# Performance work log

Hardware: AMD Instinct MI355X
Metric: run time of the kernel (lower is better)

Reference implementation:

```python
import jax, jax.numpy as jnp
import numpy as np

N_NODES = 100000
N_EDGES = 1600000
D_FEAT = 64


def setup_inputs() -> dict:
    key = jax.random.key(0)
    k1, k2, k3 = jax.random.split(key, 3)
    h = jax.random.normal(k1, (N_NODES, D_FEAT), dtype=jnp.float32)
    src = jax.random.randint(k2, (N_EDGES,), 0, N_NODES, dtype=jnp.int32)
    dst = jax.random.randint(k3, (N_EDGES,), 0, N_NODES, dtype=jnp.int32)
    edge_index = jnp.stack([src, dst], axis=0)  # [2, E]
    return {"h": h, "edge_index": edge_index}


def reference(h, edge_index):
    # EdgePassing: message = src node features (gather along edges)
    # Max_aggregation: per-dst-node max over incoming messages (segment max)
    src, dst = edge_index[0], edge_index[1]
    msgs = h[src]  # [E, D] gathered mailbox, never densified per-node
    agg = jax.ops.segment_max(msgs, dst, num_segments=N_NODES)  # [N, D]
    # DGL leaves nodes with no incoming messages at zero; segment_max yields -inf
    return jnp.where(jnp.isneginf(agg), jnp.zeros_like(agg), agg)
```

## Files before the change

### kernel.cpp

```cpp
#include <hip/hip_runtime.h>
#include <stdint.h>

#define D_FEAT 64
#define NEG_INF_BITS 0xFF800000u
#define ENC_NEG_INF  0x007FFFFFu
#define NPB 64
#define BSHIFT 6
#define BM_BLOCK 256
#define MAXB 2048
#define PL_BLOCKS 256
#define PL_THREADS 1024
#define O_CAP 65536

__device__ __forceinline__ unsigned enc_f32(float v) {
    unsigned b = __float_as_uint(v);
    return ((int)b >= 0) ? (b ^ 0x80000000u) : ~b;
}
__device__ __forceinline__ unsigned dec_bits(unsigned u) {
    if (u == ENC_NEG_INF) return 0u;
    return (u & 0x80000000u) ? (u ^ 0x80000000u) : ~u;
}

__global__ void __launch_bounds__(PL_THREADS)
place_kernel(const int* __restrict__ src, const int* __restrict__ dst,
             int* __restrict__ cnt, int* __restrict__ ovf_cnt,
             int* __restrict__ ovf_dst, int* __restrict__ ovf_src,
             unsigned* __restrict__ packed,
             int E, int Te, int B, int cap, int aligned4) {
    __shared__ int lh[MAXB];
    int t = blockIdx.x;
    int beg = t * Te;
    int end = min(E, beg + Te);
    if (beg >= end) return;
    for (int i = threadIdx.x; i < B; i += blockDim.x) lh[i] = 0;
    __syncthreads();
    int nE = end - beg;
    int n4 = aligned4 ? (nE >> 2) : 0;
    const int4* d4 = (const int4*)(dst + beg);
    for (int k = threadIdx.x; k < n4; k += blockDim.x) {
        int4 d = d4[k];
        atomicAdd(&lh[d.x >> BSHIFT], 1);
        atomicAdd(&lh[d.y >> BSHIFT], 1);
        atomicAdd(&lh[d.z >> BSHIFT], 1);
        atomicAdd(&lh[d.w >> BSHIFT], 1);
    }
    for (int i = beg + (n4 << 2) + threadIdx.x; i < end; i += blockDim.x)
        atomicAdd(&lh[dst[i] >> BSHIFT], 1);
    __syncthreads();
    for (int i = threadIdx.x; i < B; i += blockDim.x) {
        int c = lh[i];
        lh[i] = c ? atomicAdd(&cnt[i], c) : 0;
    }
    __syncthreads();
    for (int i = beg + threadIdx.x; i < end; i += blockDim.x) {
        int d = dst[i];
        int s = src[i];
        int b = d >> BSHIFT;
        int pos = atomicAdd(&lh[b], 1);
        if (pos < cap) {
            packed[(size_t)b * cap + pos] = (unsigned)s | ((unsigned)(d & (NPB - 1)) << 17);
        } else {
            int o = atomicAdd(ovf_cnt, 1);
            if (o < O_CAP) { ovf_dst[o] = d; ovf_src[o] = s; }
        }
    }
}

__global__ void __launch_bounds__(BM_BLOCK)
bucket_max_kernel(const float* __restrict__ h,
                  const int* __restrict__ cnt, const int* __restrict__ ovf_cnt,
                  const int* __restrict__ ovf_dst, const int* __restrict__ ovf_src,
                  const int* __restrict__ src, const int* __restrict__ dst,
                  const unsigned* __restrict__ packed,
                  float* __restrict__ out, int N, int E, int cap) {
    __shared__ unsigned buf[NPB * D_FEAT];
    int b = blockIdx.x;
    int tid = threadIdx.x;
    int node0 = b << BSHIFT;
    int nvals = (min(NPB, N - node0)) * D_FEAT;

    for (int i = tid; i < NPB * D_FEAT; i += BM_BLOCK) buf[i] = ENC_NEG_INF;
    __syncthreads();

    int total = cnt[b];
    int beg = b * cap;
    int end = beg + min(total, cap);
    int wid = tid >> 6;
    int lane = tid & 63;

    for (int base = beg + (wid << 6); base < end; base += BM_BLOCK) {
        int nk = min(64, end - base);
        unsigned p = (lane < nk) ? packed[base + lane] : 0u;
        int j = 0;
        for (; j + 8 <= nk; j += 8) {
            unsigned q[8];
            float v[8];
            #pragma unroll
            for (int k = 0; k < 8; ++k) q[k] = (unsigned)__shfl((int)p, j + k);
            #pragma unroll
            for (int k = 0; k < 8; ++k) v[k] = h[(size_t)(q[k] & 0x1FFFFu) * D_FEAT + lane];
            #pragma unroll
            for (int k = 0; k < 8; ++k)
                atomicMax(&buf[(q[k] >> 17) * D_FEAT + lane], enc_f32(v[k]));
        }
        for (; j < nk; ++j) {
            unsigned pj = (unsigned)__shfl((int)p, j);
            float v = h[(size_t)(pj & 0x1FFFFu) * D_FEAT + lane];
            atomicMax(&buf[(pj >> 17) * D_FEAT + lane], enc_f32(v));
        }
    }

    int ov = *ovf_cnt;
    if (ov > 0) {
        if (ov <= O_CAP) {
            for (int i = 0; i < ov; ++i) {
                int d = ovf_dst[i];
                if ((d >> BSHIFT) == b) {
                    float v = h[(size_t)ovf_src[i] * D_FEAT + lane];
                    atomicMax(&buf[(d & (NPB - 1)) * D_FEAT + lane], enc_f32(v));
                }
            }
        } else if (total > cap) {
            for (int e = tid; e < E; e += BM_BLOCK) {
                int d = dst[e];
                if ((d >> BSHIFT) == b) {
                    const float* hr = h + (size_t)src[e] * D_FEAT;
                    int row = (d & (NPB - 1)) * D_FEAT;
                    for (int f = 0; f < D_FEAT; ++f)
                        atomicMax(&buf[row + f], enc_f32(hr[f]));
                }
            }
        }
    }
    __syncthreads();

    if (nvals == NPB * D_FEAT) {
        uint4* o4 = (uint4*)(out + (size_t)node0 * D_FEAT);
        const uint4* b4 = (const uint4*)buf;
        for (int i = tid; i < (NPB * D_FEAT) / 4; i += BM_BLOCK) {
            uint4 u = b4[i];
            uint4 r;
            r.x = dec_bits(u.x); r.y = dec_bits(u.y);
            r.z = dec_bits(u.z); r.w = dec_bits(u.w);
            o4[i] = r;
        }
    } else {
        unsigned* o = (unsigned*)(out + (size_t)node0 * D_FEAT);
        for (int i = tid; i < nvals; i += BM_BLOCK) o[i] = dec_bits(buf[i]);
    }
}

__global__ void init_out_kernel(uint4* __restrict__ out, int n4) {
    int i = blockIdx.x * blockDim.x + threadIdx.x;
    if (i < n4) {
        uint4 v;
        v.x = NEG_INF_BITS; v.y = NEG_INF_BITS; v.z = NEG_INF_BITS; v.w = NEG_INF_BITS;
        out[i] = v;
    }
}
__global__ void scatter_max_kernel(const float* __restrict__ h, const int* __restrict__ src,
                                   const int* __restrict__ dst, float* __restrict__ out, int E) {
    int gid = blockIdx.x * blockDim.x + threadIdx.x;
    int e = gid >> 6;
    if (e >= E) return;
    int lane = gid & 63;
    float v = h[src[e] * D_FEAT + lane];
    int* addr = (int*)(out + dst[e] * D_FEAT + lane);
    if (v >= 0.0f) atomicMax(addr, __float_as_int(v));
    else           atomicMin((unsigned int*)addr, __float_as_uint(v));
}
__global__ void finalize_kernel(float* __restrict__ out, int n) {
    int i = blockIdx.x * blockDim.x + threadIdx.x;
    if (i < n && __float_as_uint(out[i]) == NEG_INF_BITS) out[i] = 0.0f;
}

extern "C" void kernel_launch(void* const* d_in, const int* in_sizes, int n_in,
                              void* d_out, int out_size, void* d_ws, size_t ws_size,
                              hipStream_t stream) {
    const float* h = (const float*)d_in[0];
    const int* edge_index = (const int*)d_in[1];
    int E = in_sizes[1] / 2;
    const int* src = edge_index;
    const int* dst = edge_index + E;
    float* out = (float*)d_out;
    int N = out_size / D_FEAT;

    int B = (N + NPB - 1) >> BSHIFT;

    int cap = 0;
    if (B > 0) {
        cap = (((E / B) * 5) / 4 + 63) & ~63;
        if (cap < 128) cap = 128;
    }
    size_t need = ((size_t)B + 1 + 2 * (size_t)O_CAP + (size_t)B * cap) * sizeof(int);

    if (N <= (1 << 17) && B <= MAXB && E > 0 && cap > 0 && ws_size >= need) {
        int* cnt         = (int*)d_ws;
        int* ovf_cnt     = cnt + B;
        int* ovf_dst     = ovf_cnt + 1;
        int* ovf_src     = ovf_dst + O_CAP;
        unsigned* packed = (unsigned*)(ovf_src + O_CAP);

        int aligned4 = (((((uintptr_t)dst) | ((uintptr_t)src)) & 15) == 0) ? 1 : 0;

        hipMemsetAsync(cnt, 0, (size_t)(B + 1) * sizeof(int), stream);

        int Te = ((E + PL_BLOCKS - 1) / PL_BLOCKS + 3) & ~3;
        place_kernel<<<PL_BLOCKS, PL_THREADS, 0, stream>>>(
            src, dst, cnt, ovf_cnt, ovf_dst, ovf_src, packed, E, Te, B, cap, aligned4);

        bucket_max_kernel<<<B, BM_BLOCK, 0, stream>>>(
            h, cnt, ovf_cnt, ovf_dst, ovf_src, src, dst, packed, out, N, E, cap);
    } else {
        int n4 = out_size / 4;
        init_out_kernel<<<(n4 + 255) / 256, 256, 0, stream>>>((uint4*)out, n4);
        long long total = (long long)E * 64;
        scatter_max_kernel<<<(int)((total + 255) / 256), 256, 0, stream>>>(h, src, dst, out, E);
        finalize_kernel<<<(out_size + 255) / 256, 256, 0, stream>>>(out, out_size);
    }
}
```

Baseline: 155.8 us.

## Pad per-block bucket reservations to 16 entries and cut placement blocks to 64

Each placement block now reserves bucket slots rounded up to multiples of 16 and fills the unused tail with a sentinel. Writes into the packed edge list therefore land in aligned, contiguous 64-byte runs per block rather than scattered single words. Using fewer placement blocks (64 instead of 256) keeps the padding overhead bounded, and the bucket capacity is enlarged to absorb it. The max kernel skips sentinel entries. The cost is more workspace, extra sentinel writes, a branch in the hot gather loop, and less parallelism in the placement pass.

Result: slower. 234.5 us (+50.5%).

```diff
diff --git a/kernel.cpp b/kernel.cpp
--- a/kernel.cpp
+++ b/kernel.cpp
@@ -4,11 +4,14 @@
 #define D_FEAT 64
 #define NEG_INF_BITS 0xFF800000u
 #define ENC_NEG_INF  0x007FFFFFu
+#define SENTINEL     0xFFFFFFFFu
 #define NPB 64
 #define BSHIFT 6
 #define BM_BLOCK 256
 #define MAXB 2048
-#define PL_BLOCKS 256
+#define PAD 16
+#define PL_BLOCKS_PAD 64
+#define PL_BLOCKS_STD 256
 #define PL_THREADS 1024
 #define O_CAP 65536
 
@@ -26,42 +29,58 @@
              int* __restrict__ cnt, int* __restrict__ ovf_cnt,
              int* __restrict__ ovf_dst, int* __restrict__ ovf_src,
              unsigned* __restrict__ packed,
-             int E, int Te, int B, int cap, int aligned4) {
-    __shared__ int lh[MAXB];
+             int E, int Te, int B, int cap, int aligned4, int pad) {
+    __shared__ int lcnt[MAXB];
+    __shared__ int lcur[MAXB];
     int t = blockIdx.x;
     int beg = t * Te;
     int end = min(E, beg + Te);
     if (beg >= end) return;
-    for (int i = threadIdx.x; i < B; i += blockDim.x) lh[i] = 0;
+    for (int i = threadIdx.x; i < B; i += blockDim.x) lcnt[i] = 0;
     __syncthreads();
     int nE = end - beg;
     int n4 = aligned4 ? (nE >> 2) : 0;
     const int4* d4 = (const int4*)(dst + beg);
     for (int k = threadIdx.x; k < n4; k += blockDim.x) {
         int4 d = d4[k];
-        atomicAdd(&lh[d.x >> BSHIFT], 1);
-        atomicAdd(&lh[d.y >> BSHIFT], 1);
-        atomicAdd(&lh[d.z >> BSHIFT], 1);
-        atomicAdd(&lh[d.w >> BSHIFT], 1);
+        atomicAdd(&lcnt[d.x >> BSHIFT], 1);
+        atomicAdd(&lcnt[d.y >> BSHIFT], 1);
+        atomicAdd(&lcnt[d.z >> BSHIFT], 1);
+        atomicAdd(&lcnt[d.w >> BSHIFT], 1);
     }
     for (int i = beg + (n4 << 2) + threadIdx.x; i < end; i += blockDim.x)
-        atomicAdd(&lh[dst[i] >> BSHIFT], 1);
+        atomicAdd(&lcnt[dst[i] >> BSHIFT], 1);
     __syncthreads();
     for (int i = threadIdx.x; i < B; i += blockDim.x) {
-        int c = lh[i];
-        lh[i] = c ? atomicAdd(&cnt[i], c) : 0;
+        int c = lcnt[i];
+        int res = (pad > 1) ? ((c + pad - 1) & ~(pad - 1)) : c;
+        lcur[i] = c ? atomicAdd(&cnt[i], res) : 0;
     }
     __syncthreads();
     for (int i = beg + threadIdx.x; i < end; i += blockDim.x) {
         int d = dst[i];
         int s = src[i];
         int b = d >> BSHIFT;
-        int pos = atomicAdd(&lh[b], 1);
+        int pos = atomicAdd(&lcur[b], 1);
         if (pos < cap) {
             packed[(size_t)b * cap + pos] = (unsigned)s | ((unsigned)(d & (NPB - 1)) << 17);
         } else {
             int o = atomicAdd(ovf_cnt, 1);
             if (o < O_CAP) { ovf_dst[o] = d; ovf_src[o] = s; }
+        }
+    }
+    if (pad > 1) {
+        __syncthreads();
+        for (int i = threadIdx.x; i < B; i += blockDim.x) {
+            int c = lcnt[i];
+            if (c) {
+                int curv = lcur[i];
+                int base = curv - c;
+                int endp = base + ((c + pad - 1) & ~(pad - 1));
+                int fe = min(endp, cap);
+                for (int s2 = curv; s2 < fe; ++s2)
+                    packed[(size_t)i * cap + s2] = SENTINEL;
+            }
         }
     }
 }
@@ -90,23 +109,26 @@
 
     for (int base = beg + (wid << 6); base < end; base += BM_BLOCK) {
         int nk = min(64, end - base);
-        unsigned p = (lane < nk) ? packed[base + lane] : 0u;
+        unsigned p = (lane < nk) ? packed[base + lane] : SENTINEL;
         int j = 0;
         for (; j + 8 <= nk; j += 8) {
             unsigned q[8];
-            float v[8];
             #pragma unroll
             for (int k = 0; k < 8; ++k) q[k] = (unsigned)__shfl((int)p, j + k);
             #pragma unroll
-            for (int k = 0; k < 8; ++k) v[k] = h[(size_t)(q[k] & 0x1FFFFu) * D_FEAT + lane];
-            #pragma unroll
-            for (int k = 0; k < 8; ++k)
-                atomicMax(&buf[(q[k] >> 17) * D_FEAT + lane], enc_f32(v[k]));
+            for (int k = 0; k < 8; ++k) {
+                if (q[k] != SENTINEL) {
+                    float v = h[(size_t)(q[k] & 0x1FFFFu) * D_FEAT + lane];
+                    atomicMax(&buf[(q[k] >> 17) * D_FEAT + lane], enc_f32(v));
+                }
+            }
         }
         for (; j < nk; ++j) {
             unsigned pj = (unsigned)__shfl((int)p, j);
-            float v = h[(size_t)(pj & 0x1FFFFu) * D_FEAT + lane];
-            atomicMax(&buf[(pj >> 17) * D_FEAT + lane], enc_f32(v));
+            if (pj != SENTINEL) {
+                float v = h[(size_t)(pj & 0x1FFFFu) * D_FEAT + lane];
+                atomicMax(&buf[(pj >> 17) * D_FEAT + lane], enc_f32(v));
+            }
         }
     }
 
@@ -187,35 +209,44 @@
 
     int B = (N + NPB - 1) >> BSHIFT;
 
-    int cap = 0;
-    if (B > 0) {
-        cap = (((E / B) * 5) / 4 + 63) & ~63;
-        if (cap < 128) cap = 128;
-    }
-    size_t need = ((size_t)B + 1 + 2 * (size_t)O_CAP + (size_t)B * cap) * sizeof(int);
-
-    if (N <= (1 << 17) && B <= MAXB && E > 0 && cap > 0 && ws_size >= need) {
-        int* cnt         = (int*)d_ws;
-        int* ovf_cnt     = cnt + B;
-        int* ovf_dst     = ovf_cnt + 1;
-        int* ovf_src     = ovf_dst + O_CAP;
-        unsigned* packed = (unsigned*)(ovf_src + O_CAP);
-
-        int aligned4 = (((((uintptr_t)dst) | ((uintptr_t)src)) & 15) == 0) ? 1 : 0;
-
-        hipMemsetAsync(cnt, 0, (size_t)(B + 1) * sizeof(int), stream);
-
-        int Te = ((E + PL_BLOCKS - 1) / PL_BLOCKS + 3) & ~3;
-        place_kernel<<<PL_BLOCKS, PL_THREADS, 0, stream>>>(
-            src, dst, cnt, ovf_cnt, ovf_dst, ovf_src, packed, E, Te, B, cap, aligned4);
-
-        bucket_max_kernel<<<B, BM_BLOCK, 0, stream>>>(
-            h, cnt, ovf_cnt, ovf_dst, ovf_src, src, dst, packed, out, N, E, cap);
-    } else {
-        int n4 = out_size / 4;
-        init_out_kernel<<<(n4 + 255) / 256, 256, 0, stream>>>((uint4*)out, n4);
-        long long total = (long long)E * 64;
-        scatter_max_kernel<<<(int)((total + 255) / 256), 256, 0, stream>>>(h, src, dst, out, E);
-        finalize_kernel<<<(out_size + 255) / 256, 256, 0, stream>>>(out, out_size);
-    }
-}
+    if (N <= (1 << 17) && B <= MAXB && E > 0) {
+        int meanb = E / B;
+        int capP = (((meanb + PL_BLOCKS_PAD * 10) * 5) / 4 + 63) & ~63;
+        if (capP < 128) capP = 128;
+        size_t needP = ((size_t)B + 1 + 2 * (size_t)O_CAP + (size_t)B * capP) * sizeof(int);
+        int cap0 = ((meanb * 5) / 4 + 63) & ~63;
+        if (cap0 < 128) cap0 = 128;
+        size_t need0 = ((size_t)B + 1 + 2 * (size_t)O_CAP + (size_t)B * cap0) * sizeof(int);
+
+        int use_pad = (ws_size >= needP) ? 1 : 0;
+        int cap = use_pad ? capP : cap0;
+        size_t need = use_pad ? needP : need0;
+
+        if (ws_size >= need) {
+            int* cnt         = (int*)d_ws;
+            int* ovf_cnt     = cnt + B;
+            int* ovf_dst     = ovf_cnt + 1;
+            int* ovf_src     = ovf_dst + O_CAP;
+            unsigned* packed = (unsigned*)(ovf_src + O_CAP);
+
+            int aligned4 = (((((uintptr_t)dst) | ((uintptr_t)src)) & 15) == 0) ? 1 : 0;
+
+            hipMemsetAsync(cnt, 0, (size_t)(B + 1) * sizeof(int), stream);
+
+            int pl_blocks = use_pad ? PL_BLOCKS_PAD : PL_BLOCKS_STD;
+            int pad       = use_pad ? PAD : 1;
+            int Te = ((E + pl_blocks - 1) / pl_blocks + 3) & ~3;
+            place_kernel<<<pl_blocks, PL_THREADS, 0, stream>>>(
+                src, dst, cnt, ovf_cnt, ovf_dst, ovf_src, packed, E, Te, B, cap, aligned4, pad);
+
+            bucket_max_kernel<<<B, BM_BLOCK, 0, stream>>>(
+                h, cnt, ovf_cnt, ovf_dst, ovf_src, src, dst, packed, out, N, E, cap);
+            return;
+        }
+    }
+    int n4 = out_size / 4;
+    init_out_kernel<<<(n4 + 255) / 256, 256, 0, stream>>>((uint4*)out, n4);
+    long long total = (long long)E * 64;
+    scatter_max_kernel<<<(int)((total + 255) / 256), 256, 0, stream>>>(h, src, dst, out, E);
+    finalize_kernel<<<(out_size + 255) / 256, 256, 0, stream>>>(out, out_size);
+}
```

## Stage bucketed edges in shared memory for coalesced scatter writes

Applied to the files above, without the earlier changes.

The placement kernel now processes fixed 4096-edge chunks with 512 threads per block instead of 256 large blocks. Each block computes a local exclusive scan over its per-bucket counts. It writes packed edges into shared memory sorted by bucket, then streams them out in rank order, so global writes to each bucket's slot range are contiguous rather than scattered. This adds a block-wide scan, extra barriers and more shared-memory use, and launches about 391 blocks, each doing a B-wide histogram clear and atomics.

Result: slower. 176.3 us (+13.1%).

```diff
diff --git a/kernel.cpp b/kernel.cpp
--- a/kernel.cpp
+++ b/kernel.cpp
@@ -8,8 +8,8 @@
 #define BSHIFT 6
 #define BM_BLOCK 256
 #define MAXB 2048
-#define PL_BLOCKS 256
-#define PL_THREADS 1024
+#define CH 4096
+#define PL_THREADS 512
 #define O_CAP 65536
 
 __device__ __forceinline__ unsigned enc_f32(float v) {
@@ -26,43 +26,88 @@
              int* __restrict__ cnt, int* __restrict__ ovf_cnt,
              int* __restrict__ ovf_dst, int* __restrict__ ovf_src,
              unsigned* __restrict__ packed,
-             int E, int Te, int B, int cap, int aligned4) {
+             int E, int B, int cap, int aligned4) {
     __shared__ int lh[MAXB];
-    int t = blockIdx.x;
-    int beg = t * Te;
-    int end = min(E, beg + Te);
+    __shared__ int lo[MAXB];
+    __shared__ int gb[MAXB];
+    __shared__ unsigned sval[CH];
+    __shared__ int sdel[CH];
+    const int tid = threadIdx.x;
+    const int t = blockIdx.x;
+    int beg = t * CH;
+    int end = min(E, beg + CH);
     if (beg >= end) return;
-    for (int i = threadIdx.x; i < B; i += blockDim.x) lh[i] = 0;
-    __syncthreads();
     int nE = end - beg;
+
+    for (int i = tid; i < B; i += PL_THREADS) lh[i] = 0;
+    __syncthreads();
     int n4 = aligned4 ? (nE >> 2) : 0;
     const int4* d4 = (const int4*)(dst + beg);
-    for (int k = threadIdx.x; k < n4; k += blockDim.x) {
+    for (int k = tid; k < n4; k += PL_THREADS) {
         int4 d = d4[k];
         atomicAdd(&lh[d.x >> BSHIFT], 1);
         atomicAdd(&lh[d.y >> BSHIFT], 1);
         atomicAdd(&lh[d.z >> BSHIFT], 1);
         atomicAdd(&lh[d.w >> BSHIFT], 1);
     }
-    for (int i = beg + (n4 << 2) + threadIdx.x; i < end; i += blockDim.x)
+    for (int i = beg + (n4 << 2) + tid; i < end; i += PL_THREADS)
         atomicAdd(&lh[dst[i] >> BSHIFT], 1);
     __syncthreads();
-    for (int i = threadIdx.x; i < B; i += blockDim.x) {
-        int c = lh[i];
-        lh[i] = c ? atomicAdd(&cnt[i], c) : 0;
-    }
-    __syncthreads();
-    for (int i = beg + threadIdx.x; i < end; i += blockDim.x) {
+
+    int i0 = tid << 2;
+    int c0 = 0, c1 = 0, c2 = 0, c3 = 0;
+    if (i0 + 0 < B) c0 = lh[i0 + 0];
+    if (i0 + 1 < B) c1 = lh[i0 + 1];
+    if (i0 + 2 < B) c2 = lh[i0 + 2];
+    if (i0 + 3 < B) c3 = lh[i0 + 3];
+    int s = c0 + c1 + c2 + c3;
+    int* scr = sdel;
+    scr[tid] = s;
+    __syncthreads();
+    for (int off = 1; off < PL_THREADS; off <<= 1) {
+        int v = (tid >= off) ? scr[tid - off] : 0;
+        __syncthreads();
+        scr[tid] += v;
+        __syncthreads();
+    }
+    int excl = scr[tid] - s;
+    {
+        int e0 = excl;
+        if (i0 + 0 < B) { lo[i0+0] = e0; if (c0) gb[i0+0] = (i0+0)*cap + atomicAdd(&cnt[i0+0], c0) - e0; }
+        e0 += c0;
+        if (i0 + 1 < B) { lo[i0+1] = e0; if (c1) gb[i0+1] = (i0+1)*cap + atomicAdd(&cnt[i0+1], c1) - e0; }
+        e0 += c1;
+        if (i0 + 2 < B) { lo[i0+2] = e0; if (c2) gb[i0+2] = (i0+2)*cap + atomicAdd(&cnt[i0+2], c2) - e0; }
+        e0 += c2;
+        if (i0 + 3 < B) { lo[i0+3] = e0; if (c3) gb[i0+3] = (i0+3)*cap + atomicAdd(&cnt[i0+3], c3) - e0; }
+    }
+    __syncthreads();
+
+    for (int i = tid; i < B; i += PL_THREADS) lh[i] = 0;
+    __syncthreads();
+
+    for (int i = beg + tid; i < end; i += PL_THREADS) {
         int d = dst[i];
-        int s = src[i];
+        int sv = src[i];
         int b = d >> BSHIFT;
-        int pos = atomicAdd(&lh[b], 1);
-        if (pos < cap) {
-            packed[(size_t)b * cap + pos] = (unsigned)s | ((unsigned)(d & (NPB - 1)) << 17);
+        unsigned val = (unsigned)sv | ((unsigned)(d & (NPB - 1)) << 17);
+        int rank = atomicAdd(&lh[b], 1);
+        int r = lo[b] + rank;
+        sval[r] = val;
+        int gslot = gb[b] + r - b * cap;
+        if (gslot < cap) {
+            sdel[r] = gb[b];
         } else {
+            sdel[r] = INT32_MIN;
             int o = atomicAdd(ovf_cnt, 1);
-            if (o < O_CAP) { ovf_dst[o] = d; ovf_src[o] = s; }
-        }
+            if (o < O_CAP) { ovf_dst[o] = d; ovf_src[o] = sv; }
+        }
+    }
+    __syncthreads();
+
+    for (int r = tid; r < nE; r += PL_THREADS) {
+        int del = sdel[r];
+        if (del != INT32_MIN) packed[(size_t)(del + r)] = sval[r];
     }
 }
 
@@ -205,9 +250,9 @@
 
         hipMemsetAsync(cnt, 0, (size_t)(B + 1) * sizeof(int), stream);
 
-        int Te = ((E + PL_BLOCKS - 1) / PL_BLOCKS + 3) & ~3;
-        place_kernel<<<PL_BLOCKS, PL_THREADS, 0, stream>>>(
-            src, dst, cnt, ovf_cnt, ovf_dst, ovf_src, packed, E, Te, B, cap, aligned4);
+        int pl_blocks = (E + CH - 1) / CH;
+        place_kernel<<<pl_blocks, PL_THREADS, 0, stream>>>(
+            src, dst, cnt, ovf_cnt, ovf_dst, ovf_src, packed, E, B, cap, aligned4);
 
         bucket_max_kernel<<<B, BM_BLOCK, 0, stream>>>(
             h, cnt, ovf_cnt, ovf_dst, ovf_src, src, dst, packed, out, N, E, cap);
```
